# Kernel optimization log

Hardware: AMD Instinct MI355X
Metric: run time of the kernel (lower is better)

## Reference

```python
import jax, jax.numpy as jnp
import numpy as np

N_EMBD = 1568  # 2 * 784
EPS = 1e-5


def layernorm(x, g, b):
    mu = jnp.mean(x, axis=-1, keepdims=True)
    var = jnp.var(x, axis=-1, keepdims=True)
    return (x - mu) * jax.lax.rsqrt(var + EPS) * g + b


def setup_inputs() -> dict:
    key = jax.random.key(0)
    ks = jax.random.split(key, 8)
    B, D, H, HS, FF, OUT = 1024, N_EMBD, 16, 98, 4 * N_EMBD, N_EMBD // 2
    s = 0.02
    return {
        "x": jax.random.normal(ks[0], (B, D), jnp.float32),
        "Wq": jax.random.normal(ks[1], (H, D, HS), jnp.float32) * s,
        "Wk": jax.random.normal(ks[2], (H, D, HS), jnp.float32) * s,
        "Wv": jax.random.normal(ks[3], (H, D, HS), jnp.float32) * s,
        "Wo": jax.random.normal(ks[4], (D, D), jnp.float32) * s,
        "bo": jnp.zeros((D,), jnp.float32),
        "g1": jnp.ones((D,), jnp.float32),
        "b1": jnp.zeros((D,), jnp.float32),
        "g2": jnp.ones((D,), jnp.float32),
        "b2": jnp.zeros((D,), jnp.float32),
        "W1": jax.random.normal(ks[5], (D, FF), jnp.float32) * s,
        "b1f": jnp.zeros((FF,), jnp.float32),
        "W2": jax.random.normal(ks[6], (FF, OUT), jnp.float32) * s,
        "b2f": jnp.zeros((OUT,), jnp.float32),
    }


def reference(x, Wq, Wk, Wv, Wo, bo, g1, b1, g2, b2, W1, b1f, W2, b2f):
    B, D = x.shape
    h = layernorm(x, g1, b1)                       # (B, D)
    # all 16 heads batched: per-head QKV projections
    q = jnp.einsum('bd,hde->bhe', h, Wq)           # (B, H, 98)
    k = jnp.einsum('bd,hde->bhe', h, Wk)
    v = jnp.einsum('bd,hde->bhe', h, Wv)
    # outer-product pseudo-attention, scaled by N**-0.5 with N = n_embd
    attn = jnp.einsum('bhi,bhj->bhij', q, k) * (D ** -0.5)  # (B, H, 98, 98)
    attn = jax.nn.softmax(attn, axis=-1)
    out = jnp.einsum('bhij,bhj->bhi', attn, v)     # (B, H, 98)
    out = out.reshape(B, D)                        # concat heads
    out = out @ Wo + bo                            # output proj (dropout = identity in eval)
    h2 = layernorm(out, g2, b2)
    ff = jax.nn.gelu(h2 @ W1 + b1f, approximate=False) @ W2 + b2f  # (B, 784)
    return ff
```

## Files before the change

### kernel.cpp

```cpp
#include <hip/hip_runtime.h>
#include <math.h>

#define B_ROWS 1024
#define D_EMB  1568
#define KP     1600
#define H_HEADS 16
#define HSZ    98
#define FF_DIM 6272
#define OUT_DIM 784

typedef unsigned short ushort_t;
typedef __attribute__((ext_vector_type(8))) short short8;
typedef __attribute__((ext_vector_type(4))) float floatx4;

static __device__ __forceinline__ ushort_t f2bf(float f) {
    unsigned int u = __builtin_bit_cast(unsigned int, f);
    u = (u + 0x7fffu + ((u >> 16) & 1u)) >> 16;
    return (ushort_t)u;
}
static __device__ __forceinline__ float bf2f(ushort_t h) {
    unsigned int u = ((unsigned int)h) << 16;
    return __builtin_bit_cast(float, u);
}

static __device__ __forceinline__ void load16_to_lds(const void* g, void* l) {
    __builtin_amdgcn_global_load_lds(
        (const __attribute__((address_space(1))) void*)g,
        (__attribute__((address_space(3))) void*)l,
        16, 0, 0);
}

__global__ __launch_bounds__(256) void ln_kernel(const float* __restrict__ x,
                                                 const float* __restrict__ g,
                                                 const float* __restrict__ b,
                                                 ushort_t* __restrict__ out,
                                                 int D, int DPAD) {
    const int row = blockIdx.x;
    const float* xr = x + (size_t)row * D;
    ushort_t* orow = out + (size_t)row * DPAD;

    float s = 0.f, s2 = 0.f;
    for (int i = threadIdx.x; i < D; i += blockDim.x) {
        float v = xr[i];
        s += v; s2 += v * v;
    }
    #pragma unroll
    for (int off = 32; off > 0; off >>= 1) {
        s  += __shfl_down(s,  off, 64);
        s2 += __shfl_down(s2, off, 64);
    }
    __shared__ float ws_[8], ws2_[8];
    const int wave = threadIdx.x >> 6, lane = threadIdx.x & 63;
    if (lane == 0) { ws_[wave] = s; ws2_[wave] = s2; }
    __syncthreads();
    if (threadIdx.x == 0) {
        float ts = 0.f, ts2 = 0.f;
        for (int i = 0; i < 4; i++) { ts += ws_[i]; ts2 += ws2_[i]; }
        ws_[0] = ts; ws2_[0] = ts2;
    }
    __syncthreads();
    const float mean = ws_[0] / (float)D;
    const float var  = ws2_[0] / (float)D - mean * mean;
    const float inv  = rsqrtf(var + 1e-5f);
    for (int i = threadIdx.x; i < DPAD; i += blockDim.x)
        orow[i] = (i < D) ? f2bf((xr[i] - mean) * inv * g[i] + b[i]) : (ushort_t)0;
}

__global__ __launch_bounds__(256) void transpose_plain(const float* __restrict__ src,
                                                       ushort_t* __restrict__ dst,
                                                       int K, int N, int Npad, int dstride) {
    __shared__ float t[64][65];
    const int n0 = blockIdx.x * 64, k0 = blockIdx.y * 64;
    const int tid = threadIdx.x;
    const int tx = tid & 63, ty = tid >> 6;
    #pragma unroll
    for (int r = 0; r < 16; r++) {
        const int kl = ty + r * 4;
        const int k = k0 + kl, n = n0 + tx;
        t[tx][kl] = (k < K && n < N) ? src[(size_t)k * N + n] : 0.f;
    }
    __syncthreads();
    #pragma unroll
    for (int w = 0; w < 4; w++) {
        const int nl = (tid >> 4) + w * 16;
        const int kc = (tid & 15) * 4;
        const int n = n0 + nl, k = k0 + kc;
        if (n < Npad && k < K) {
            ushort4 uv;
            uv.x = f2bf(t[nl][kc + 0]);
            uv.y = f2bf(t[nl][kc + 1]);
            uv.z = f2bf(t[nl][kc + 2]);
            uv.w = f2bf(t[nl][kc + 3]);
            *(ushort4*)(dst + (size_t)n * dstride + k) = uv;
        }
    }
}

__global__ __launch_bounds__(256) void transpose_qkv(const float* __restrict__ Wq,
                                                     const float* __restrict__ Wk,
                                                     const float* __restrict__ Wv,
                                                     ushort_t* __restrict__ dst, int K) {
    __shared__ float t[32][33];
    const int which = blockIdx.z >> 4;
    const int head  = blockIdx.z & 15;
    const float* src = (which == 0) ? Wq : (which == 1) ? Wk : Wv;
    src += (size_t)head * K * HSZ;
    const int e0 = blockIdx.x * 32, k0 = blockIdx.y * 32;
    const int tx = threadIdx.x, ty = threadIdx.y;
    #pragma unroll
    for (int i = 0; i < 4; i++) {
        const int k = k0 + ty + i * 8, e = e0 + tx;
        t[ty + i * 8][tx] = (e < HSZ && k < K) ? src[(size_t)k * HSZ + e] : 0.f;
    }
    __syncthreads();
    const int nbase = which * D_EMB + head * HSZ;
    #pragma unroll
    for (int i = 0; i < 4; i++) {
        const int e = e0 + ty + i * 8, k = k0 + tx;
        if (e < HSZ && k < K) dst[(size_t)(nbase + e) * KP + k] = f2bf(t[tx][ty + i * 8]);
    }
}

__global__ __launch_bounds__(256) void gemm_bf16(const ushort_t* __restrict__ A,
                                                 const ushort_t* __restrict__ Bt,
                                                 ushort_t* __restrict__ P,
                                                 int N, int Kstride, int nkTot) {
    __shared__ __align__(16) ushort_t As[2 * 128 * 32];
    __shared__ __align__(16) ushort_t Bs[2 * 128 * 32];

    const int tid  = threadIdx.x;
    const int wave = tid >> 6, lane = tid & 63;
    const int quad = lane >> 4, l16 = lane & 15;
    const int m0 = blockIdx.x * 128;
    const int n0 = blockIdx.y * 128;
    const int z = blockIdx.z, Z = gridDim.z;
    const int it0 = (int)((long long)nkTot * z / Z);
    const int it1 = (int)((long long)nkTot * (z + 1) / Z);

    const int srow = lane >> 2;
    const int scol = (lane & 3) << 3;
    const int wm = wave & 1, wn = wave >> 1;

    floatx4 acc[4][4] = {};

    for (int it = it0; it < it1; ++it) {
        const int k0 = it << 6;
        #pragma unroll
        for (int c = 0; c < 2; ++c) {
            const int rg = wave * 2 + c;
            const int row = rg * 16 + srow;
            #pragma unroll
            for (int ks = 0; ks < 2; ++ks) {
                load16_to_lds(A  + (size_t)(m0 + row) * Kstride + k0 + ks * 32 + scol,
                              &As[ks * 4096 + rg * 512]);
                load16_to_lds(Bt + (size_t)(n0 + row) * Kstride + k0 + ks * 32 + scol,
                              &Bs[ks * 4096 + rg * 512]);
            }
        }
        __syncthreads();

        #pragma unroll
        for (int ks = 0; ks < 2; ++ks) {
            short8 af[4], bfr[4];
            #pragma unroll
            for (int i = 0; i < 4; i++)
                af[i] = *(const short8*)&As[ks * 4096 + (wm * 64 + i * 16 + l16) * 32 + quad * 8];
            #pragma unroll
            for (int j = 0; j < 4; j++)
                bfr[j] = *(const short8*)&Bs[ks * 4096 + (wn * 64 + j * 16 + l16) * 32 + quad * 8];
            #pragma unroll
            for (int i = 0; i < 4; i++)
                #pragma unroll
                for (int j = 0; j < 4; j++)
                    acc[i][j] = __builtin_amdgcn_mfma_f32_16x16x32_bf16(af[i], bfr[j], acc[i][j], 0, 0, 0);
        }
        __syncthreads();
    }

    ushort_t* Pz = P + (size_t)z * B_ROWS * N;
    #pragma unroll
    for (int i = 0; i < 4; i++) {
        const int rbase = m0 + wm * 64 + i * 16 + quad * 4;
        #pragma unroll
        for (int j = 0; j < 4; j++) {
            const int col = n0 + wn * 64 + j * 16 + l16;
            if (col < N) {
                #pragma unroll
                for (int r = 0; r < 4; r++)
                    Pz[(size_t)(rbase + r) * N + col] = f2bf(acc[i][j][r]);
            }
        }
    }
}

template <int Z>
__global__ __launch_bounds__(256) void combine_ln_kernel(const ushort_t* __restrict__ P,
                                                         const float* __restrict__ bias,
                                                         const float* __restrict__ g,
                                                         const float* __restrict__ b,
                                                         ushort_t* __restrict__ out,
                                                         int N, int NPAD) {
    __shared__ float t[D_EMB];
    __shared__ float ws_[8], ws2_[8];
    const int row = blockIdx.x;
    const size_t plane = (size_t)B_ROWS * N;
    const ushort_t* Pr = P + (size_t)row * N;
    const int half = N >> 1;

    float s = 0.f, s2 = 0.f;
    for (int i = threadIdx.x; i < half; i += blockDim.x) {
        float v0 = bias[2 * i], v1 = bias[2 * i + 1];
        #pragma unroll
        for (int zz = 0; zz < Z; zz++) {
            const ushort2 u = *(const ushort2*)(Pr + (size_t)zz * plane + 2 * i);
            v0 += bf2f(u.x); v1 += bf2f(u.y);
        }
        t[2 * i] = v0; t[2 * i + 1] = v1;
        s += v0 + v1; s2 += v0 * v0 + v1 * v1;
    }
    #pragma unroll
    for (int off = 32; off > 0; off >>= 1) {
        s  += __shfl_down(s,  off, 64);
        s2 += __shfl_down(s2, off, 64);
    }
    const int wave = threadIdx.x >> 6, lane = threadIdx.x & 63;
    if (lane == 0) { ws_[wave] = s; ws2_[wave] = s2; }
    __syncthreads();
    if (threadIdx.x == 0) {
        float ts = 0.f, ts2 = 0.f;
        for (int i = 0; i < 4; i++) { ts += ws_[i]; ts2 += ws2_[i]; }
        ws_[0] = ts; ws2_[0] = ts2;
    }
    __syncthreads();
    const float mean = ws_[0] / (float)N;
    const float var  = ws2_[0] / (float)N - mean * mean;
    const float inv  = rsqrtf(var + 1e-5f);
    ushort_t* orow = out + (size_t)row * NPAD;
    for (int i = threadIdx.x; i < NPAD; i += blockDim.x)
        orow[i] = (i < N) ? f2bf((t[i] - mean) * inv * g[i] + b[i]) : (ushort_t)0;
}

__global__ __launch_bounds__(256) void combine_gelu_kernel(ushort_t* __restrict__ P,
                                                           const float* __restrict__ bias,
                                                           int N) {
    const int c4 = (blockIdx.x * 256 + threadIdx.x) * 4;
    if (c4 >= N) return;
    const int row = blockIdx.y;
    const size_t plane = (size_t)B_ROWS * N;
    const size_t off = (size_t)row * N + c4;
    const ushort4 a = *(const ushort4*)(P + off);
    const ushort4 c = *(const ushort4*)(P + plane + off);
    float v[4] = { bf2f(a.x) + bf2f(c.x) + bias[c4 + 0],
                   bf2f(a.y) + bf2f(c.y) + bias[c4 + 1],
                   bf2f(a.z) + bf2f(c.z) + bias[c4 + 2],
                   bf2f(a.w) + bf2f(c.w) + bias[c4 + 3] };
    ushort4 o;
    #pragma unroll
    for (int j = 0; j < 4; j++)
        v[j] = 0.5f * v[j] * (1.f + erff(v[j] * 0.70710678118654752f));
    o.x = f2bf(v[0]); o.y = f2bf(v[1]); o.z = f2bf(v[2]); o.w = f2bf(v[3]);
    *(ushort4*)(P + off) = o;
}

template <int Z>
__global__ __launch_bounds__(256) void combine_out_kernel(const ushort_t* __restrict__ P,
                                                          const float* __restrict__ bias,
                                                          float* __restrict__ out, int N) {
    const int c2 = blockIdx.x * 256 + threadIdx.x;
    if (c2 >= (N >> 1)) return;
    const int row = blockIdx.y;
    const size_t plane = (size_t)B_ROWS * N;
    const size_t off = (size_t)row * N + 2 * c2;
    float v0 = bias[2 * c2], v1 = bias[2 * c2 + 1];
    #pragma unroll
    for (int zz = 0; zz < Z; zz++) {
        const ushort2 u = *(const ushort2*)(P + (size_t)zz * plane + off);
        v0 += bf2f(u.x); v1 += bf2f(u.y);
    }
    out[off] = v0; out[off + 1] = v1;
}

__global__ __launch_bounds__(128) void attn_kernel(const ushort_t* __restrict__ P,
                                                   ushort_t* __restrict__ out) {
    const int bh = blockIdx.x;
    const int b = bh >> 4, h = bh & 15;
    const size_t base = (size_t)b * 4704 + h * HSZ;
    const size_t plane = (size_t)B_ROWS * 4704;

    __shared__ float ks[HSZ], vs[HSZ];
    __shared__ float kmax_s, kmin_s;

    const int t = threadIdx.x;
    if (t < HSZ) {
        ks[t] = bf2f(P[base + 1568 + t]) + bf2f(P[plane + base + 1568 + t]);
        vs[t] = bf2f(P[base + 3136 + t]) + bf2f(P[plane + base + 3136 + t]);
    }
    __syncthreads();
    if (t == 0) {
        float mx = -1e30f, mn = 1e30f;
        for (int j = 0; j < HSZ; j++) { mx = fmaxf(mx, ks[j]); mn = fminf(mn, ks[j]); }
        kmax_s = mx; kmin_s = mn;
    }
    __syncthreads();
    if (t < HSZ) {
        const float q = bf2f(P[base + t]) + bf2f(P[plane + base + t]);
        const float ti = q * 0.025253813613805268f;
        const float m = (ti >= 0.f) ? ti * kmax_s : ti * kmin_s;
        float s = 0.f, acc = 0.f;
        for (int j = 0; j < HSZ; j++) {
            const float e = __expf(ti * ks[j] - m);
            s += e; acc += e * vs[j];
        }
        out[(size_t)b * KP + h * HSZ + t] = f2bf(acc / s);
    }
}

extern "C" void kernel_launch(void* const* d_in, const int* in_sizes, int n_in,
                              void* d_out, int out_size, void* d_ws, size_t ws_size,
                              hipStream_t stream) {
    const float* x   = (const float*)d_in[0];
    const float* Wq  = (const float*)d_in[1];
    const float* Wk  = (const float*)d_in[2];
    const float* Wv  = (const float*)d_in[3];
    const float* Wo  = (const float*)d_in[4];
    const float* bo  = (const float*)d_in[5];
    const float* g1  = (const float*)d_in[6];
    const float* b1  = (const float*)d_in[7];
    const float* g2  = (const float*)d_in[8];
    const float* b2  = (const float*)d_in[9];
    const float* W1  = (const float*)d_in[10];
    const float* b1f = (const float*)d_in[11];
    const float* W2  = (const float*)d_in[12];
    const float* b2f = (const float*)d_in[13];
    float* out = (float*)d_out;

    char* w = (char*)d_ws;
    ushort_t* qkvt = (ushort_t*)(w);
    ushort_t* Wot  = (ushort_t*)(w + 15155200);
    ushort_t* W1t  = (ushort_t*)(w);
    ushort_t* W2t  = (ushort_t*)(w);
    ushort_t* Pb   = (ushort_t*)(w + 20480000);
    ushort_t* ff1  = Pb;
    ushort_t* Pw2  = (ushort_t*)(w + 33325056);
    ushort_t* h_bf = (ushort_t*)(w + 47775744);

    ln_kernel<<<B_ROWS, 256, 0, stream>>>(x, g1, b1, h_bf, D_EMB, KP);

    transpose_qkv<<<dim3(4, 49, 48), dim3(32, 8), 0, stream>>>(Wq, Wk, Wv, qkvt, D_EMB);
    transpose_plain<<<dim3(26, 25), 256, 0, stream>>>(Wo, Wot, D_EMB, D_EMB, 1664, KP);

    gemm_bf16<<<dim3(8, 37, 2), 256, 0, stream>>>(h_bf, qkvt, Pb, 4704, KP, 25);

    attn_kernel<<<B_ROWS * H_HEADS, 128, 0, stream>>>(Pb, h_bf);

    gemm_bf16<<<dim3(8, 13, 6), 256, 0, stream>>>(h_bf, Wot, Pb, D_EMB, KP, 25);

    transpose_plain<<<dim3(98, 25), 256, 0, stream>>>(W1, W1t, D_EMB, FF_DIM, FF_DIM, KP);

    combine_ln_kernel<6><<<B_ROWS, 256, 0, stream>>>(Pb, bo, g2, b2, h_bf, D_EMB, KP);

    gemm_bf16<<<dim3(8, 49, 2), 256, 0, stream>>>(h_bf, W1t, Pb, FF_DIM, KP, 25);

    transpose_plain<<<dim3(14, 98), 256, 0, stream>>>(W2, W2t, FF_DIM, OUT_DIM, 896, FF_DIM);

    combine_gelu_kernel<<<dim3(7, B_ROWS), 256, 0, stream>>>(Pb, b1f, FF_DIM);

    gemm_bf16<<<dim3(8, 7, 9), 256, 0, stream>>>(ff1, W2t, Pw2, OUT_DIM, FF_DIM, 98);

    combine_out_kernel<9><<<dim3(2, B_ROWS), 256, 0, stream>>>(Pw2, b2f, out, OUT_DIM);
}
```

Measured before the change: 372.6 us.

## Merge weight transposes into two prep kernels and fuse bias+GELU into FFN GEMM

Weight transposes are merged into two launches: QKV with Wo, and W1 with W2. The QKV transpose now uses the 64x64 tile path. The first FFN GEMM drops split-K and applies bias plus exact GELU in its epilogue, which removes the separate combine_gelu pass and one partial plane of traffic. The output-projection split-K drops from 6 to 4, and the workspace layout is reshuffled so W2t and Pw2 no longer overlap live buffers. The cost is fewer blocks in the W1 GEMM (392 blocks) and erf work in the GEMM epilogue.

```diff
diff --git a/kernel.cpp b/kernel.cpp
--- a/kernel.cpp
+++ b/kernel.cpp
@@ -66,18 +66,20 @@
         orow[i] = (i < D) ? f2bf((xr[i] - mean) * inv * g[i] + b[i]) : (ushort_t)0;
 }
 
-__global__ __launch_bounds__(256) void transpose_plain(const float* __restrict__ src,
-                                                       ushort_t* __restrict__ dst,
-                                                       int K, int N, int Npad, int dstride) {
+static __device__ __forceinline__ void transpose_tile(const float* __restrict__ src,
+                                                      ushort_t* __restrict__ dst,
+                                                      int srcN, int Kvalid,
+                                                      int k0, int n0,
+                                                      int Nvalid, int Npad,
+                                                      int dstride, int dbase) {
     __shared__ float t[64][65];
-    const int n0 = blockIdx.x * 64, k0 = blockIdx.y * 64;
     const int tid = threadIdx.x;
     const int tx = tid & 63, ty = tid >> 6;
     #pragma unroll
     for (int r = 0; r < 16; r++) {
         const int kl = ty + r * 4;
         const int k = k0 + kl, n = n0 + tx;
-        t[tx][kl] = (k < K && n < N) ? src[(size_t)k * N + n] : 0.f;
+        t[tx][kl] = (k < Kvalid && n < Nvalid) ? src[(size_t)k * srcN + n] : 0.f;
     }
     __syncthreads();
     #pragma unroll
@@ -85,45 +87,68 @@
         const int nl = (tid >> 4) + w * 16;
         const int kc = (tid & 15) * 4;
         const int n = n0 + nl, k = k0 + kc;
-        if (n < Npad && k < K) {
+        if (n < Npad && k < Kvalid) {
             ushort4 uv;
             uv.x = f2bf(t[nl][kc + 0]);
             uv.y = f2bf(t[nl][kc + 1]);
             uv.z = f2bf(t[nl][kc + 2]);
             uv.w = f2bf(t[nl][kc + 3]);
-            *(ushort4*)(dst + (size_t)n * dstride + k) = uv;
-        }
-    }
-}
-
-__global__ __launch_bounds__(256) void transpose_qkv(const float* __restrict__ Wq,
-                                                     const float* __restrict__ Wk,
-                                                     const float* __restrict__ Wv,
-                                                     ushort_t* __restrict__ dst, int K) {
-    __shared__ float t[32][33];
-    const int which = blockIdx.z >> 4;
-    const int head  = blockIdx.z & 15;
-    const float* src = (which == 0) ? Wq : (which == 1) ? Wk : Wv;
-    src += (size_t)head * K * HSZ;
-    const int e0 = blockIdx.x * 32, k0 = blockIdx.y * 32;
-    const int tx = threadIdx.x, ty = threadIdx.y;
-    #pragma unroll
-    for (int i = 0; i < 4; i++) {
-        const int k = k0 + ty + i * 8, e = e0 + tx;
-        t[ty + i * 8][tx] = (e < HSZ && k < K) ? src[(size_t)k * HSZ + e] : 0.f;
-    }
-    __syncthreads();
-    const int nbase = which * D_EMB + head * HSZ;
-    #pragma unroll
-    for (int i = 0; i < 4; i++) {
-        const int e = e0 + ty + i * 8, k = k0 + tx;
-        if (e < HSZ && k < K) dst[(size_t)(nbase + e) * KP + k] = f2bf(t[tx][ty + i * 8]);
-    }
-}
-
+            *(ushort4*)(dst + (size_t)(dbase + n) * dstride + k) = uv;
+        }
+    }
+}
+
+__global__ __launch_bounds__(256) void prep1_kernel(const float* __restrict__ Wq,
+                                                    const float* __restrict__ Wk,
+                                                    const float* __restrict__ Wv,
+                                                    const float* __restrict__ Wo,
+                                                    ushort_t* __restrict__ qkvt,
+                                                    ushort_t* __restrict__ Wot) {
+    const int id = blockIdx.x;
+    if (id < 2400) {
+        const int ktile = id % 25;
+        const int rest  = id / 25;
+        const int ntile = rest & 1;
+        const int hw    = rest >> 1;
+        const int head  = hw & 15;
+        const int which = hw >> 4;
+        const float* src = (which == 0) ? Wq : (which == 1) ? Wk : Wv;
+        src += (size_t)head * D_EMB * HSZ;
+        transpose_tile(src, qkvt, HSZ, D_EMB, ktile * 64, ntile * 64,
+                       HSZ, HSZ, KP, which * D_EMB + head * HSZ);
+    } else {
+        const int id2 = id - 2400;
+        const int ktile = id2 % 25;
+        const int ntile = id2 / 25;
+        transpose_tile(Wo, Wot, D_EMB, D_EMB, ktile * 64, ntile * 64,
+                       D_EMB, 1664, KP, 0);
+    }
+}
+
+__global__ __launch_bounds__(256) void prep2_kernel(const float* __restrict__ W1,
+                                                    const float* __restrict__ W2,
+                                                    ushort_t* __restrict__ W1t,
+                                                    ushort_t* __restrict__ W2t) {
+    const int id = blockIdx.x;
+    if (id < 2450) {
+        const int ktile = id % 25;
+        const int ntile = id / 25;
+        transpose_tile(W1, W1t, FF_DIM, D_EMB, ktile * 64, ntile * 64,
+                       FF_DIM, FF_DIM, KP, 0);
+    } else {
+        const int id2 = id - 2450;
+        const int ktile = id2 % 98;
+        const int ntile = id2 / 98;
+        transpose_tile(W2, W2t, OUT_DIM, FF_DIM, ktile * 64, ntile * 64,
+                       OUT_DIM, 896, FF_DIM, 0);
+    }
+}
+
+template <int EPI>
 __global__ __launch_bounds__(256) void gemm_bf16(const ushort_t* __restrict__ A,
                                                  const ushort_t* __restrict__ Bt,
                                                  ushort_t* __restrict__ P,
+                                                 const float* __restrict__ bias,
                                                  int N, int Kstride, int nkTot) {
     __shared__ __align__(16) ushort_t As[2 * 128 * 32];
     __shared__ __align__(16) ushort_t Bs[2 * 128 * 32];
@@ -177,7 +202,7 @@
         __syncthreads();
     }
 
-    ushort_t* Pz = P + (size_t)z * B_ROWS * N;
+    ushort_t* Pz = (EPI == 0) ? (P + (size_t)z * B_ROWS * N) : P;
     #pragma unroll
     for (int i = 0; i < 4; i++) {
         const int rbase = m0 + wm * 64 + i * 16 + quad * 4;
@@ -186,8 +211,14 @@
             const int col = n0 + wn * 64 + j * 16 + l16;
             if (col < N) {
                 #pragma unroll
-                for (int r = 0; r < 4; r++)
-                    Pz[(size_t)(rbase + r) * N + col] = f2bf(acc[i][j][r]);
+                for (int r = 0; r < 4; r++) {
+                    float v = acc[i][j][r];
+                    if (EPI == 1) {
+                        v += bias[col];
+                        v = 0.5f * v * (1.f + erff(v * 0.70710678118654752f));
+                    }
+                    Pz[(size_t)(rbase + r) * N + col] = f2bf(v);
+                }
             }
         }
     }
@@ -238,28 +269,6 @@
     ushort_t* orow = out + (size_t)row * NPAD;
     for (int i = threadIdx.x; i < NPAD; i += blockDim.x)
         orow[i] = (i < N) ? f2bf((t[i] - mean) * inv * g[i] + b[i]) : (ushort_t)0;
-}
-
-__global__ __launch_bounds__(256) void combine_gelu_kernel(ushort_t* __restrict__ P,
-                                                           const float* __restrict__ bias,
-                                                           int N) {
-    const int c4 = (blockIdx.x * 256 + threadIdx.x) * 4;
-    if (c4 >= N) return;
-    const int row = blockIdx.y;
-    const size_t plane = (size_t)B_ROWS * N;
-    const size_t off = (size_t)row * N + c4;
-    const ushort4 a = *(const ushort4*)(P + off);
-    const ushort4 c = *(const ushort4*)(P + plane + off);
-    float v[4] = { bf2f(a.x) + bf2f(c.x) + bias[c4 + 0],
-                   bf2f(a.y) + bf2f(c.y) + bias[c4 + 1],
-                   bf2f(a.z) + bf2f(c.z) + bias[c4 + 2],
-                   bf2f(a.w) + bf2f(c.w) + bias[c4 + 3] };
-    ushort4 o;
-    #pragma unroll
-    for (int j = 0; j < 4; j++)
-        v[j] = 0.5f * v[j] * (1.f + erff(v[j] * 0.70710678118654752f));
-    o.x = f2bf(v[0]); o.y = f2bf(v[1]); o.z = f2bf(v[2]); o.w = f2bf(v[3]);
-    *(ushort4*)(P + off) = o;
 }
 
 template <int Z>
@@ -338,34 +347,29 @@
     ushort_t* qkvt = (ushort_t*)(w);
     ushort_t* Wot  = (ushort_t*)(w + 15155200);
     ushort_t* W1t  = (ushort_t*)(w);
-    ushort_t* W2t  = (ushort_t*)(w);
+    ushort_t* Pw2  = (ushort_t*)(w);
     ushort_t* Pb   = (ushort_t*)(w + 20480000);
-    ushort_t* ff1  = Pb;
-    ushort_t* Pw2  = (ushort_t*)(w + 33325056);
+    ushort_t* ff1  = (ushort_t*)(w + 20480000);
+    ushort_t* W2t  = (ushort_t*)(w + 33325056);
     ushort_t* h_bf = (ushort_t*)(w + 47775744);
 
     ln_kernel<<<B_ROWS, 256, 0, stream>>>(x, g1, b1, h_bf, D_EMB, KP);
 
-    transpose_qkv<<<dim3(4, 49, 48), dim3(32, 8), 0, stream>>>(Wq, Wk, Wv, qkvt, D_EMB);
-    transpose_plain<<<dim3(26, 25), 256, 0, stream>>>(Wo, Wot, D_EMB, D_EMB, 1664, KP);
-
-    gemm_bf16<<<dim3(8, 37, 2), 256, 0, stream>>>(h_bf, qkvt, Pb, 4704, KP, 25);
+    prep1_kernel<<<3050, 256, 0, stream>>>(Wq, Wk, Wv, Wo, qkvt, Wot);
+
+    gemm_bf16<0><<<dim3(8, 37, 2), 256, 0, stream>>>(h_bf, qkvt, Pb, nullptr, 4704, KP, 25);
 
     attn_kernel<<<B_ROWS * H_HEADS, 128, 0, stream>>>(Pb, h_bf);
 
-    gemm_bf16<<<dim3(8, 13, 6), 256, 0, stream>>>(h_bf, Wot, Pb, D_EMB, KP, 25);
-
-    transpose_plain<<<dim3(98, 25), 256, 0, stream>>>(W1, W1t, D_EMB, FF_DIM, FF_DIM, KP);
-
-    combine_ln_kernel<6><<<B_ROWS, 256, 0, stream>>>(Pb, bo, g2, b2, h_bf, D_EMB, KP);
-
-    gemm_bf16<<<dim3(8, 49, 2), 256, 0, stream>>>(h_bf, W1t, Pb, FF_DIM, KP, 25);
-
-    transpose_plain<<<dim3(14, 98), 256, 0, stream>>>(W2, W2t, FF_DIM, OUT_DIM, 896, FF_DIM);
-
-    combine_gelu_kernel<<<dim3(7, B_ROWS), 256, 0, stream>>>(Pb, b1f, FF_DIM);
-
-    gemm_bf16<<<dim3(8, 7, 9), 256, 0, stream>>>(ff1, W2t, Pw2, OUT_DIM, FF_DIM, 98);
+    gemm_bf16<0><<<dim3(8, 13, 4), 256, 0, stream>>>(h_bf, Wot, Pb, nullptr, D_EMB, KP, 25);
+
+    combine_ln_kernel<4><<<B_ROWS, 256, 0, stream>>>(Pb, bo, g2, b2, h_bf, D_EMB, KP);
+
+    prep2_kernel<<<3822, 256, 0, stream>>>(W1, W2, W1t, W2t);
+
+    gemm_bf16<1><<<dim3(8, 49, 1), 256, 0, stream>>>(h_bf, W1t, ff1, b1f, FF_DIM, KP, 25);
+
+    gemm_bf16<0><<<dim3(8, 7, 9), 256, 0, stream>>>(ff1, W2t, Pw2, nullptr, OUT_DIM, FF_DIM, 98);
 
     combine_out_kernel<9><<<dim3(2, B_ROWS), 256, 0, stream>>>(Pw2, b2f, out, OUT_DIM);
 }
```

New measurement: 351.7 us. 1.06x faster.
